# Optimization experiments

Hardware: AMD Instinct MI355X
Metric: run time of the kernel (lower is better)

The kernel has to match this reference:

```python
import jax, jax.numpy as jnp
import numpy as np

WS, SHIFT, HEADS = 8, 4, 12
B, H0, W0, C, HID = 16, 64, 64, 384, 1536
EPS = 1e-5


def _rel_pos_index():
    # WindowMSA.double_step_seq(2*Ww-1, Wh, 1, Ww), then coords + coords.T, then flip(1)
    seq1 = np.arange(0, (2 * WS - 1) * WS, 2 * WS - 1)
    seq2 = np.arange(0, WS)
    coords = (seq1[:, None] + seq2[None, :]).reshape(1, -1)  # (1, N)
    idx = coords + coords.T                                   # (N, N)
    return np.ascontiguousarray(idx[:, ::-1]).reshape(-1)

REL_IDX = jnp.asarray(_rel_pos_index())


def _attn_mask(Hp, Wp):
    # Swin shift mask: region labels -> per-window pairwise (-100 where regions differ)
    img = np.zeros((Hp, Wp))
    sl = (slice(0, -WS), slice(-WS, -SHIFT), slice(-SHIFT, None))
    cnt = 0
    for hs in sl:
        for ws in sl:
            img[hs, ws] = cnt
            cnt += 1
    mw = img.reshape(Hp // WS, WS, Wp // WS, WS).transpose(0, 2, 1, 3).reshape(-1, WS * WS)
    am = mw[:, None, :] - mw[:, :, None]
    return jnp.asarray(np.where(am != 0, -100.0, 0.0), np.float32)


def _ln(z, g, b):
    m = z.mean(-1, keepdims=True)
    v = ((z - m) ** 2).mean(-1, keepdims=True)
    return (z - m) * jax.lax.rsqrt(v + EPS) * g + b


def _bn(z, g, b):
    # eval-mode BatchNorm2d with running mean=0, var=1
    scale = g * (1.0 / np.sqrt(1.0 + EPS))
    return z * scale[None, :, None, None] + b[None, :, None, None]


def setup_inputs() -> dict:
    key = jax.random.key(0)
    ks = jax.random.split(key, 8)
    p = lambda k, sh: jax.random.normal(k, sh, jnp.float32) * 0.02
    return {
        "x": jax.random.normal(ks[0], (B, H0 * W0, C), jnp.float32),
        "H": H0, "W": W0,
        "ln1_g": jnp.ones((C,), jnp.float32), "ln1_b": jnp.zeros((C,), jnp.float32),
        "qkv_w": p(ks[1], (3 * C, C)), "qkv_b": jnp.zeros((3 * C,), jnp.float32),
        "rpb_table": p(ks[2], ((2 * WS - 1) ** 2, HEADS)),
        "proj_w": p(ks[3], (C, C)), "proj_b": jnp.zeros((C,), jnp.float32),
        "ln2_g": jnp.ones((C,), jnp.float32), "ln2_b": jnp.zeros((C,), jnp.float32),
        "fc1_w": p(ks[4], (HID, C)), "fc1_b": jnp.zeros((HID,), jnp.float32),
        "bn1_g": jnp.ones((HID,), jnp.float32), "bn1_b": jnp.zeros((HID,), jnp.float32),
        "dw_w": p(ks[5], (HID, 1, 3, 3)), "dw_b": jnp.zeros((HID,), jnp.float32),
        "bn2_g": jnp.ones((HID,), jnp.float32), "bn2_b": jnp.zeros((HID,), jnp.float32),
        "fc2_w": p(ks[6], (C, HID)), "fc2_b": jnp.zeros((C,), jnp.float32),
        "bn3_g": jnp.ones((C,), jnp.float32), "bn3_b": jnp.zeros((C,), jnp.float32),
    }


def reference(x, H, W, ln1_g, ln1_b, qkv_w, qkv_b, rpb_table, proj_w, proj_b,
              ln2_g, ln2_b, fc1_w, fc1_b, bn1_g, bn1_b, dw_w, dw_b,
              bn2_g, bn2_b, fc2_w, fc2_b, bn3_g, bn3_b):
    Bx, L, Cx = x.shape
    hd = Cx // HEADS
    # ---------- shifted-window MHSA branch ----------
    h = _ln(x, ln1_g, ln1_b).reshape(Bx, H, W, Cx)
    h = jnp.roll(h, (-SHIFT, -SHIFT), axis=(1, 2))
    nH, nW = H // WS, W // WS
    N = WS * WS
    win = h.reshape(Bx, nH, WS, nW, WS, Cx).transpose(0, 1, 3, 2, 4, 5).reshape(-1, N, Cx)
    qkv = (win @ qkv_w.T + qkv_b).reshape(-1, N, 3, HEADS, hd).transpose(2, 0, 3, 1, 4)
    q, k, v = qkv[0] * (hd ** -0.5), qkv[1], qkv[2]  # (B*nW, heads, N, hd)
    attn = jnp.einsum('whnd,whmd->whnm', q, k)
    bias = rpb_table[REL_IDX].reshape(N, N, HEADS).transpose(2, 0, 1)  # (heads, N, N)
    attn = attn + bias[None]
    mask = _attn_mask(H, W)  # (num_windows, N, N)
    attn = attn.reshape(Bx, nH * nW, HEADS, N, N) + mask[None, :, None]
    attn = jax.nn.softmax(attn.reshape(-1, HEADS, N, N), axis=-1)
    out = jnp.einsum('whnm,whmd->whnd', attn, v).transpose(0, 2, 1, 3).reshape(-1, N, Cx)
    out = out @ proj_w.T + proj_b
    out = out.reshape(Bx, nH, nW, WS, WS, Cx).transpose(0, 1, 3, 2, 4, 5).reshape(Bx, H, W, Cx)
    out = jnp.roll(out, (SHIFT, SHIFT), axis=(1, 2)).reshape(Bx, L, Cx)
    x = x + out
    # ---------- MlpDWBN branch ----------
    h = _ln(x, ln2_g, ln2_b)
    z = h.transpose(0, 2, 1).reshape(Bx, Cx, H, W)
    z = jnp.einsum('oc,bchw->bohw', fc1_w, z) + fc1_b[None, :, None, None]
    z = jax.nn.gelu(_bn(z, bn1_g, bn1_b), approximate=False)
    z = jax.lax.conv_general_dilated(z, dw_w, (1, 1), 'SAME',
                                     feature_group_count=z.shape[1],
                                     dimension_numbers=('NCHW', 'OIHW', 'NCHW'))
    z = z + dw_b[None, :, None, None]
    z = jax.nn.gelu(_bn(z, bn2_g, bn2_b), approximate=False)
    z = jnp.einsum('oc,bchw->bohw', fc2_w, z) + fc2_b[None, :, None, None]
    z = jax.nn.gelu(_bn(z, bn3_g, bn3_b), approximate=False)
    z = z.reshape(Bx, Cx, -1).transpose(0, 2, 1)
    return x + z
```

## Files before the change

kernel.cpp:

```cpp
#include <hip/hip_runtime.h>
#include <cstddef>


#define CCH 384
#define HIDCH 1536

typedef __attribute__((ext_vector_type(8))) short short8;
typedef __attribute__((ext_vector_type(4))) float f32x4;

__device__ __forceinline__ float gelu_exact(float v) {
  return 0.5f * v * (1.0f + erff(v * 0.70710678118654752440f));
}
__device__ __forceinline__ unsigned short f2bf(float f) {
  unsigned u = __builtin_bit_cast(unsigned, f);
  u = (u + 0x7FFF + ((u >> 16) & 1)) >> 16;
  return (unsigned short)u;
}
__device__ __forceinline__ float bf2f(unsigned short s) {
  return __builtin_bit_cast(float, (unsigned)s << 16);
}
__device__ __forceinline__ int region_label(int p) {
  return (p < 56) ? 0 : ((p < 60) ? 1 : 2);
}

__device__ __forceinline__ void gl_lds16(const void* g, void* l) {
  __builtin_amdgcn_global_load_lds(
      (const __attribute__((address_space(1))) unsigned int*)g,
      (__attribute__((address_space(3))) unsigned int*)l, 16, 0, 0);
}

__global__ __launch_bounds__(256) void convw_kernel(
    const float* __restrict__ a, const float* __restrict__ b,
    const float* __restrict__ c, const float* __restrict__ d,
    const float* __restrict__ dww, unsigned short* __restrict__ o,
    float* __restrict__ dwt) {
  const int i = blockIdx.x * 256 + threadIdx.x;
  if (i < 1769472) {
    float v;
    if (i < 442368) v = a[i];
    else if (i < 589824) v = b[i - 442368];
    else if (i < 1179648) v = c[i - 589824];
    else v = d[i - 1179648];
    o[i] = f2bf(v);
  } else if (i < 1769472 + 13824) {
    const int j = i - 1769472;
    const int tap = j / 1536;
    const int ch = j - tap * 1536;
    dwt[j] = dww[ch * 9 + tap];
  }
}

template <int REMAP>
__global__ __launch_bounds__(256) void ln_kernel(const float* __restrict__ x,
                                                 const float* __restrict__ g,
                                                 const float* __restrict__ b,
                                                 unsigned short* __restrict__ y) {
  const int t = blockIdx.x * 4 + (threadIdx.x >> 6);
  const int lane = threadIdx.x & 63;
  size_t src;
  if (REMAP) {
    const int widx = t >> 6;
    const int n = t & 63;
    const int bb = widx >> 6;
    const int wh = (widx >> 3) & 7;
    const int ww = widx & 7;
    const int hp = wh * 8 + (n >> 3);
    const int wp = ww * 8 + (n & 7);
    const int hs = (hp + 4) & 63;
    const int wsrc = (wp + 4) & 63;
    src = (size_t)bb * 4096 + hs * 64 + wsrc;
  } else {
    src = (size_t)t;
  }
  const float* xr = x + src * CCH + lane * 6;
  const float2 p0 = *(const float2*)xr;
  const float2 p1 = *(const float2*)(xr + 2);
  const float2 p2 = *(const float2*)(xr + 4);
  float v[6] = {p0.x, p0.y, p1.x, p1.y, p2.x, p2.y};
  float s = 0.f, s2 = 0.f;
#pragma unroll
  for (int j = 0; j < 6; ++j) {
    s += v[j];
    s2 += v[j] * v[j];
  }
#pragma unroll
  for (int o = 1; o < 64; o <<= 1) {
    s += __shfl_xor(s, o);
    s2 += __shfl_xor(s2, o);
  }
  const float mean = s * (1.0f / 384.0f);
  const float var = s2 * (1.0f / 384.0f) - mean * mean;
  const float rstd = rsqrtf(var + 1e-5f);
  const float2 g0 = *(const float2*)(g + lane * 6);
  const float2 g1 = *(const float2*)(g + lane * 6 + 2);
  const float2 g2 = *(const float2*)(g + lane * 6 + 4);
  const float2 b0 = *(const float2*)(b + lane * 6);
  const float2 b1 = *(const float2*)(b + lane * 6 + 2);
  const float2 b2 = *(const float2*)(b + lane * 6 + 4);
  const float gg[6] = {g0.x, g0.y, g1.x, g1.y, g2.x, g2.y};
  const float bv[6] = {b0.x, b0.y, b1.x, b1.y, b2.x, b2.y};
  unsigned pk[3];
#pragma unroll
  for (int i = 0; i < 3; ++i) {
    const float r0 = (v[2 * i] - mean) * rstd * gg[2 * i] + bv[2 * i];
    const float r1 = (v[2 * i + 1] - mean) * rstd * gg[2 * i + 1] + bv[2 * i + 1];
    pk[i] = (unsigned)f2bf(r0) | ((unsigned)f2bf(r1) << 16);
  }
  unsigned* yo = (unsigned*)(y + (size_t)t * CCH + lane * 6);
  yo[0] = pk[0];
  yo[1] = pk[1];
  yo[2] = pk[2];
}

template <int MODE>
__global__ __launch_bounds__(512) void mfma_gemm(
    const unsigned short* __restrict__ A, const unsigned short* __restrict__ W,
    const float* __restrict__ bias, void* __restrict__ CoutV,
    const float* __restrict__ Xres, const float* __restrict__ bng,
    const float* __restrict__ bnb, int N, int K) {
  __shared__ __align__(16) char smem[32768];
  const int tid = threadIdx.x;
  const int wave = tid >> 6, lane = tid & 63;
  const int qd = lane >> 4, ln16 = lane & 15;
  const int wm = wave >> 2, wn = wave & 3;

  const int nx = gridDim.x;
  const int lid0 = blockIdx.x + blockIdx.y * nx;
  const int tot = nx * gridDim.y;
  int lid = lid0;
  if ((tot & 7) == 0) lid = (lid0 & 7) * (tot >> 3) + (lid0 >> 3);
  const int m0 = (lid % nx) * 128;
  const int n0 = (lid / nx) * 128;

  f32x4 acc[4][2];
#pragma unroll
  for (int i = 0; i < 4; ++i)
#pragma unroll
    for (int j = 0; j < 2; ++j) acc[i][j] = (f32x4){0.f, 0.f, 0.f, 0.f};

  const int r = tid >> 2;
  const int cks = ((tid & 3) ^ ((tid >> 3) & 3)) * 8;

  const unsigned short* gA = A + (size_t)(m0 + r) * K + cks;
  const unsigned short* gB = W + (size_t)(n0 + r) * K + cks;
  char* baseA = smem;
  char* baseB = smem + 16384;
  const int wofs = wave * 1024;

  const int ntk = K >> 5;
  gl_lds16(gA, baseA + wofs);
  gl_lds16(gB, baseB + wofs);

  const int sA = (qd ^ ((ln16 >> 1) & 3)) * 8;

  int cur = 0;
  for (int t = 0; t < ntk; ++t) {
    __builtin_amdgcn_s_barrier();
    __builtin_amdgcn_sched_barrier(0);
    if (t + 1 < ntk) {
      const int k1 = (t + 1) * 32;
      const int nb = cur ^ 1;
      gl_lds16(gA + k1, baseA + nb * 8192 + wofs);
      gl_lds16(gB + k1, baseB + nb * 8192 + wofs);
      asm volatile("s_waitcnt vmcnt(2)" ::: "memory");
    } else {
      asm volatile("s_waitcnt vmcnt(0)" ::: "memory");
    }
    __builtin_amdgcn_s_barrier();
    __builtin_amdgcn_sched_barrier(0);
    short8 af[4], bfr[2];
#pragma unroll
    for (int mt = 0; mt < 4; ++mt)
      af[mt] = *(const short8*)(baseA + cur * 8192 +
                                ((wm * 64 + mt * 16 + ln16) * 32 + sA) * 2);
#pragma unroll
    for (int nt2 = 0; nt2 < 2; ++nt2)
      bfr[nt2] = *(const short8*)(baseB + cur * 8192 +
                                  ((wn * 32 + nt2 * 16 + ln16) * 32 + sA) * 2);
#pragma unroll
    for (int mt = 0; mt < 4; ++mt)
#pragma unroll
      for (int nt2 = 0; nt2 < 2; ++nt2)
        acc[mt][nt2] = __builtin_amdgcn_mfma_f32_16x16x32_bf16(
            af[mt], bfr[nt2], acc[mt][nt2], 0, 0, 0);
    cur ^= 1;
  }

  const float RSQ = 0.99999500003749969f;
#pragma unroll
  for (int mt = 0; mt < 4; ++mt) {
#pragma unroll
    for (int nt2 = 0; nt2 < 2; ++nt2) {
      const int col = n0 + wn * 32 + nt2 * 16 + ln16;
      const int rbase = m0 + wm * 64 + mt * 16 + qd * 4;
#pragma unroll
      for (int rg = 0; rg < 4; ++rg) {
        const int row = rbase + rg;
        const float val = acc[mt][nt2][rg] + bias[col];
        if (MODE == 0) {
          ((unsigned short*)CoutV)[(size_t)row * N + col] = f2bf(val);
        } else if (MODE == 1) {
          const int widx = row >> 6, n = row & 63;
          const int bb = widx >> 6, wh = (widx >> 3) & 7, wwi = widx & 7;
          const int hp = wh * 8 + (n >> 3), wp = wwi * 8 + (n & 7);
          const int hh = (hp + 4) & 63, wwp = (wp + 4) & 63;
          const size_t dst = ((size_t)bb * 4096 + hh * 64 + wwp) * CCH + col;
          ((float*)CoutV)[dst] = Xres[dst] + val;
        } else {
          const float vbn = val * (bng[col] * RSQ) + bnb[col];
          const float ge = gelu_exact(vbn);
          if (MODE == 2) {
            ((unsigned short*)CoutV)[(size_t)row * N + col] = f2bf(ge);
          } else {
            float* o = (float*)CoutV + (size_t)row * N + col;
            *o = *o + ge;
          }
        }
      }
    }
  }
}

__global__ __launch_bounds__(256) void attn_kernel(
    const unsigned short* __restrict__ qkv, const float* __restrict__ rpb,
    unsigned short* __restrict__ ao) {
  __shared__ __align__(16) unsigned short Pl[4][64 * 72];
  __shared__ float Inv[4][64];
  const int wloc = blockIdx.x;
  const int wave = threadIdx.x >> 6;
  const int lane = threadIdx.x & 63;
  const int head = blockIdx.y * 4 + wave;
  const int ln16 = lane & 15, qd = lane >> 4;
  const int wpos = wloc & 63;
  const int wh = (wpos >> 3) & 7, ww = wpos & 7;
  const unsigned short* qb = qkv + (size_t)wloc * 64 * 1152 + head * 32;

  short8 aq[4], bk[4];
#pragma unroll
  for (int t = 0; t < 4; ++t) {
    aq[t] = *(const short8*)(qb + (size_t)(t * 16 + ln16) * 1152 + qd * 8);
    bk[t] = *(const short8*)(qb + (size_t)(t * 16 + ln16) * 1152 + 384 + qd * 8);
  }
  short8 av[2][2];
#pragma unroll
  for (int dt = 0; dt < 2; ++dt)
#pragma unroll
    for (int ks = 0; ks < 2; ++ks)
#pragma unroll
      for (int j = 0; j < 8; ++j)
        av[dt][ks][j] = (short)qb[(size_t)(ks * 32 + qd * 8 + j) * 1152 + 768 +
                                  dt * 16 + ln16];

  f32x4 accS[4][4];
#pragma unroll
  for (int i = 0; i < 4; ++i)
#pragma unroll
    for (int j = 0; j < 4; ++j) accS[i][j] = (f32x4){0.f, 0.f, 0.f, 0.f};
#pragma unroll
  for (int mt = 0; mt < 4; ++mt)
#pragma unroll
    for (int nt = 0; nt < 4; ++nt)
      accS[mt][nt] = __builtin_amdgcn_mfma_f32_16x16x32_bf16(
          aq[mt], bk[nt], accS[mt][nt], 0, 0, 0);

  int cmv[4], rlm[4];
#pragma unroll
  for (int nt = 0; nt < 4; ++nt) {
    const int m = nt * 16 + ln16;
    const int mf = 63 - m;
    cmv[nt] = 15 * (mf >> 3) + (mf & 7);
    rlm[nt] =
        region_label(wh * 8 + (m >> 3)) * 3 + region_label(ww * 8 + (m & 7));
  }
  const float scale = 0.17677669529663687f;
  unsigned short* pw = &Pl[wave][0];
#pragma unroll
  for (int mt = 0; mt < 4; ++mt) {
#pragma unroll
    for (int rg = 0; rg < 4; ++rg) {
      const int n = mt * 16 + qd * 4 + rg;
      const int cn = 15 * (n >> 3) + (n & 7);
      const int rln =
          region_label(wh * 8 + (n >> 3)) * 3 + region_label(ww * 8 + (n & 7));
      float vv[4];
#pragma unroll
      for (int nt = 0; nt < 4; ++nt) {
        float sv = accS[mt][nt][rg] * scale + rpb[(cn + cmv[nt]) * 12 + head];
        if (rln != rlm[nt]) sv -= 100.f;
        vv[nt] = sv;
      }
      float mx = fmaxf(fmaxf(vv[0], vv[1]), fmaxf(vv[2], vv[3]));
      mx = fmaxf(mx, __shfl_xor(mx, 1));
      mx = fmaxf(mx, __shfl_xor(mx, 2));
      mx = fmaxf(mx, __shfl_xor(mx, 4));
      mx = fmaxf(mx, __shfl_xor(mx, 8));
      float sum = 0.f;
#pragma unroll
      for (int nt = 0; nt < 4; ++nt) {
        vv[nt] = __expf(vv[nt] - mx);
        sum += vv[nt];
      }
      sum += __shfl_xor(sum, 1);
      sum += __shfl_xor(sum, 2);
      sum += __shfl_xor(sum, 4);
      sum += __shfl_xor(sum, 8);
      if (ln16 == 0) Inv[wave][n] = 1.0f / sum;
#pragma unroll
      for (int nt = 0; nt < 4; ++nt)
        pw[n * 72 + nt * 16 + ln16] = f2bf(vv[nt]);
    }
  }

  f32x4 accO[2][4];
#pragma unroll
  for (int i = 0; i < 2; ++i)
#pragma unroll
    for (int j = 0; j < 4; ++j) accO[i][j] = (f32x4){0.f, 0.f, 0.f, 0.f};
#pragma unroll
  for (int ks = 0; ks < 2; ++ks) {
    short8 pb[4];
#pragma unroll
    for (int ntile = 0; ntile < 4; ++ntile)
      pb[ntile] =
          *(const short8*)&pw[(ntile * 16 + ln16) * 72 + ks * 32 + qd * 8];
#pragma unroll
    for (int dt = 0; dt < 2; ++dt)
#pragma unroll
      for (int ntile = 0; ntile < 4; ++ntile)
        accO[dt][ntile] = __builtin_amdgcn_mfma_f32_16x16x32_bf16(
            av[dt][ks], pb[ntile], accO[dt][ntile], 0, 0, 0);
  }

  float invn[4];
#pragma unroll
  for (int ntile = 0; ntile < 4; ++ntile)
    invn[ntile] = Inv[wave][ntile * 16 + ln16];
#pragma unroll
  for (int dt = 0; dt < 2; ++dt) {
#pragma unroll
    for (int ntile = 0; ntile < 4; ++ntile) {
      const int tok = ntile * 16 + ln16;
      const int d0 = dt * 16 + qd * 4;
      uint2 st;
      st.x = (unsigned)f2bf(accO[dt][ntile][0] * invn[ntile]) |
             ((unsigned)f2bf(accO[dt][ntile][1] * invn[ntile]) << 16);
      st.y = (unsigned)f2bf(accO[dt][ntile][2] * invn[ntile]) |
             ((unsigned)f2bf(accO[dt][ntile][3] * invn[ntile]) << 16);
      *(uint2*)&ao[((size_t)wloc * 64 + tok) * CCH + head * 32 + d0] = st;
    }
  }
}

__global__ __launch_bounds__(256) void dw_kernel(
    const unsigned short* __restrict__ z1, const float* __restrict__ dwt,
    const float* __restrict__ dwb, const float* __restrict__ bn2g,
    const float* __restrict__ bn2b, unsigned short* __restrict__ z2) {
  const int g = blockIdx.x * 256 + threadIdx.x;
  const int pix = g / 192;
  const int cg = g - pix * 192;
  const int c0 = cg * 8;
  const int p = pix & 4095;
  const int h = p >> 6, w = p & 63;
  const unsigned short* zb = z1 + (size_t)(pix >> 12) * 4096 * HIDCH;

  float a[8];
  {
    const float4 b0 = *(const float4*)&dwb[c0];
    const float4 b1 = *(const float4*)&dwb[c0 + 4];
    a[0] = b0.x; a[1] = b0.y; a[2] = b0.z; a[3] = b0.w;
    a[4] = b1.x; a[5] = b1.y; a[6] = b1.z; a[7] = b1.w;
  }
#pragma unroll
  for (int dh = -1; dh <= 1; ++dh) {
    const int hh = h + dh;
    if (hh < 0 || hh > 63) continue;
#pragma unroll
    for (int dx = -1; dx <= 1; ++dx) {
      const int wn = w + dx;
      if (wn < 0 || wn > 63) continue;
      const int tap = (dh + 1) * 3 + (dx + 1);
      const int4 zv = *(const int4*)&zb[((size_t)hh * 64 + wn) * HIDCH + c0];
      const float* wp = &dwt[tap * HIDCH + c0];
      const float4 w0 = *(const float4*)wp;
      const float4 w1 = *(const float4*)(wp + 4);
      a[0] += bf2f((unsigned short)(zv.x & 0xFFFF)) * w0.x;
      a[1] += bf2f((unsigned short)(((unsigned)zv.x) >> 16)) * w0.y;
      a[2] += bf2f((unsigned short)(zv.y & 0xFFFF)) * w0.z;
      a[3] += bf2f((unsigned short)(((unsigned)zv.y) >> 16)) * w0.w;
      a[4] += bf2f((unsigned short)(zv.z & 0xFFFF)) * w1.x;
      a[5] += bf2f((unsigned short)(((unsigned)zv.z) >> 16)) * w1.y;
      a[6] += bf2f((unsigned short)(zv.w & 0xFFFF)) * w1.z;
      a[7] += bf2f((unsigned short)(((unsigned)zv.w) >> 16)) * w1.w;
    }
  }
  const float RSQ = 0.99999500003749969f;
  const float4 g0 = *(const float4*)&bn2g[c0];
  const float4 g1 = *(const float4*)&bn2g[c0 + 4];
  const float4 bb0 = *(const float4*)&bn2b[c0];
  const float4 bb1 = *(const float4*)&bn2b[c0 + 4];
  const float gs[8] = {g0.x, g0.y, g0.z, g0.w, g1.x, g1.y, g1.z, g1.w};
  const float bs[8] = {bb0.x, bb0.y, bb0.z, bb0.w, bb1.x, bb1.y, bb1.z, bb1.w};
  unsigned pk[4];
#pragma unroll
  for (int i = 0; i < 4; ++i) {
    const float v0 = gelu_exact(a[2 * i] * (gs[2 * i] * RSQ) + bs[2 * i]);
    const float v1 =
        gelu_exact(a[2 * i + 1] * (gs[2 * i + 1] * RSQ) + bs[2 * i + 1]);
    pk[i] = (unsigned)f2bf(v0) | ((unsigned)f2bf(v1) << 16);
  }
  int4 st;
  st.x = pk[0]; st.y = pk[1]; st.z = pk[2]; st.w = pk[3];
  *(int4*)&z2[(size_t)pix * HIDCH + c0] = st;
}

extern "C" void kernel_launch(void* const* d_in, const int* in_sizes, int n_in,
                              void* d_out, int out_size, void* d_ws,
                              size_t ws_size, hipStream_t stream) {
  const float* x = (const float*)d_in[0];
  const float* ln1_g = (const float*)d_in[3];
  const float* ln1_b = (const float*)d_in[4];
  const float* qkv_w = (const float*)d_in[5];
  const float* qkv_b = (const float*)d_in[6];
  const float* rpb = (const float*)d_in[7];
  const float* proj_w = (const float*)d_in[8];
  const float* proj_b = (const float*)d_in[9];
  const float* ln2_g = (const float*)d_in[10];
  const float* ln2_b = (const float*)d_in[11];
  const float* fc1_w = (const float*)d_in[12];
  const float* fc1_b = (const float*)d_in[13];
  const float* bn1_g = (const float*)d_in[14];
  const float* bn1_b = (const float*)d_in[15];
  const float* dw_w = (const float*)d_in[16];
  const float* dw_b = (const float*)d_in[17];
  const float* bn2_g = (const float*)d_in[18];
  const float* bn2_b = (const float*)d_in[19];
  const float* fc2_w = (const float*)d_in[20];
  const float* fc2_b = (const float*)d_in[21];
  const float* bn3_g = (const float*)d_in[22];
  const float* bn3_b = (const float*)d_in[23];
  float* out = (float*)d_out;

  char* ws = (char*)d_ws;
  unsigned short* wsA = (unsigned short*)ws;
  unsigned short* wsAO = (unsigned short*)(ws + 50331648);
  unsigned short* wsQ = (unsigned short*)(ws + 100663296);
  unsigned short* wbf = (unsigned short*)(ws + 150994944);
  float* dwt = (float*)(ws + 154533888);
  unsigned short* w_qkv = wbf;
  unsigned short* w_proj = wbf + 442368;
  unsigned short* w_fc1 = wbf + 589824;
  unsigned short* w_fc2 = wbf + 1179648;

  convw_kernel<<<6966, 256, 0, stream>>>(qkv_w, proj_w, fc1_w, fc2_w, dw_w,
                                         wbf, dwt);
  ln_kernel<1><<<16384, 256, 0, stream>>>(x, ln1_g, ln1_b, wsA);
  for (int cb = 0; cb < 4; ++cb) {
    mfma_gemm<0><<<dim3(128, 9), 512, 0, stream>>>(
        wsA + (size_t)cb * 16384 * CCH, w_qkv, qkv_b, wsQ, nullptr, nullptr,
        nullptr, 1152, CCH);
    attn_kernel<<<dim3(256, 3), 256, 0, stream>>>(
        wsQ, rpb, wsAO + (size_t)cb * 16384 * CCH);
  }
  mfma_gemm<1><<<dim3(512, 3), 512, 0, stream>>>(wsAO, w_proj, proj_b, out, x,
                                                 nullptr, nullptr, CCH, CCH);
  ln_kernel<0><<<16384, 256, 0, stream>>>(out, ln2_g, ln2_b, wsA);
  for (int cb = 0; cb < 4; ++cb) {
    mfma_gemm<2><<<dim3(128, 12), 512, 0, stream>>>(
        wsA + (size_t)cb * 16384 * CCH, w_fc1, fc1_b, wsAO, nullptr, bn1_g,
        bn1_b, HIDCH, CCH);
    dw_kernel<<<12288, 256, 0, stream>>>(wsAO, dwt, dw_b, bn2_g, bn2_b, wsQ);
    mfma_gemm<3><<<dim3(128, 3), 512, 0, stream>>>(
        wsQ, w_fc2, fc2_b, out + (size_t)cb * 16384 * CCH, nullptr, bn3_g,
        bn3_b, CCH, HIDCH);
  }
}
```

Baseline: 1.071 ms.

## Fuse proj GEMM with residual and LayerNorm2; deepen GEMM K-step to 64

Replaces the separate projection GEMM and the second LayerNorm kernel with a single kernel. Each block computes 64 full rows of 384 outputs, adds the residual, reduces row statistics across waves through shared memory, and writes both the fp32 output and the bf16 normalized activations. This removes one full read of the activation tensor and one kernel launch. Separately, the generic MFMA GEMM now stages K=64 per iteration with a 64KB double-buffered LDS and a new XOR swizzle, halving the number of barrier rounds. In exchange, the larger LDS footprint may lower occupancy, and the LN variance is computed as E[x²]−mean², which is less numerically robust.

```diff
diff --git a/kernel.cpp b/kernel.cpp
--- a/kernel.cpp
+++ b/kernel.cpp
@@ -116,9 +116,9 @@
 __global__ __launch_bounds__(512) void mfma_gemm(
     const unsigned short* __restrict__ A, const unsigned short* __restrict__ W,
     const float* __restrict__ bias, void* __restrict__ CoutV,
-    const float* __restrict__ Xres, const float* __restrict__ bng,
-    const float* __restrict__ bnb, int N, int K) {
-  __shared__ __align__(16) char smem[32768];
+    const float* __restrict__ bng, const float* __restrict__ bnb, int N,
+    int K) {
+  __shared__ __align__(16) char smem[65536];
   const int tid = threadIdx.x;
   const int wave = tid >> 6, lane = tid & 63;
   const int qd = lane >> 4, ln16 = lane & 15;
@@ -138,51 +138,63 @@
 #pragma unroll
     for (int j = 0; j < 2; ++j) acc[i][j] = (f32x4){0.f, 0.f, 0.f, 0.f};
 
-  const int r = tid >> 2;
-  const int cks = ((tid & 3) ^ ((tid >> 3) & 3)) * 8;
-
-  const unsigned short* gA = A + (size_t)(m0 + r) * K + cks;
-  const unsigned short* gB = W + (size_t)(n0 + r) * K + cks;
-  char* baseA = smem;
-  char* baseB = smem + 16384;
+  const int rowg = tid >> 3;
+  const int cswz = ((tid & 7) ^ (rowg & 7)) * 8;
+  const unsigned short* gA = A + (size_t)(m0 + rowg) * K + cswz;
+  const unsigned short* gB = W + (size_t)(n0 + rowg) * K + cswz;
+  const size_t rstep = (size_t)64 * K;
   const int wofs = wave * 1024;
 
-  const int ntk = K >> 5;
-  gl_lds16(gA, baseA + wofs);
-  gl_lds16(gB, baseB + wofs);
-
-  const int sA = (qd ^ ((ln16 >> 1) & 3)) * 8;
+  const int ntk = K >> 6;
+  gl_lds16(gA, smem + wofs);
+  gl_lds16(gA + rstep, smem + 8192 + wofs);
+  gl_lds16(gB, smem + 16384 + wofs);
+  gl_lds16(gB + rstep, smem + 24576 + wofs);
 
   int cur = 0;
   for (int t = 0; t < ntk; ++t) {
     __builtin_amdgcn_s_barrier();
     __builtin_amdgcn_sched_barrier(0);
     if (t + 1 < ntk) {
-      const int k1 = (t + 1) * 32;
-      const int nb = cur ^ 1;
-      gl_lds16(gA + k1, baseA + nb * 8192 + wofs);
-      gl_lds16(gB + k1, baseB + nb * 8192 + wofs);
-      asm volatile("s_waitcnt vmcnt(2)" ::: "memory");
+      const int k1 = (t + 1) * 64;
+      char* nb = smem + (cur ^ 1) * 32768;
+      gl_lds16(gA + k1, nb + wofs);
+      gl_lds16(gA + rstep + k1, nb + 8192 + wofs);
+      gl_lds16(gB + k1, nb + 16384 + wofs);
+      gl_lds16(gB + rstep + k1, nb + 24576 + wofs);
+      asm volatile("s_waitcnt vmcnt(4)" ::: "memory");
     } else {
       asm volatile("s_waitcnt vmcnt(0)" ::: "memory");
     }
     __builtin_amdgcn_s_barrier();
     __builtin_amdgcn_sched_barrier(0);
-    short8 af[4], bfr[2];
-#pragma unroll
-    for (int mt = 0; mt < 4; ++mt)
-      af[mt] = *(const short8*)(baseA + cur * 8192 +
-                                ((wm * 64 + mt * 16 + ln16) * 32 + sA) * 2);
-#pragma unroll
-    for (int nt2 = 0; nt2 < 2; ++nt2)
-      bfr[nt2] = *(const short8*)(baseB + cur * 8192 +
-                                  ((wn * 32 + nt2 * 16 + ln16) * 32 + sA) * 2);
-#pragma unroll
-    for (int mt = 0; mt < 4; ++mt)
-#pragma unroll
-      for (int nt2 = 0; nt2 < 2; ++nt2)
-        acc[mt][nt2] = __builtin_amdgcn_mfma_f32_16x16x32_bf16(
-            af[mt], bfr[nt2], acc[mt][nt2], 0, 0, 0);
+    const char* bA = smem + cur * 32768;
+    const char* bB = bA + 16384;
+    short8 af[4][2], bfr[2][2];
+#pragma unroll
+    for (int mt = 0; mt < 4; ++mt) {
+      const int row = wm * 64 + mt * 16 + ln16;
+#pragma unroll
+      for (int kk = 0; kk < 2; ++kk)
+        af[mt][kk] = *(const short8*)(bA + row * 128 +
+                                      (((kk << 2) + qd) ^ (ln16 & 7)) * 16);
+    }
+#pragma unroll
+    for (int nt2 = 0; nt2 < 2; ++nt2) {
+      const int row = wn * 32 + nt2 * 16 + ln16;
+#pragma unroll
+      for (int kk = 0; kk < 2; ++kk)
+        bfr[nt2][kk] = *(const short8*)(bB + row * 128 +
+                                        (((kk << 2) + qd) ^ (ln16 & 7)) * 16);
+    }
+#pragma unroll
+    for (int kk = 0; kk < 2; ++kk)
+#pragma unroll
+      for (int mt = 0; mt < 4; ++mt)
+#pragma unroll
+        for (int nt2 = 0; nt2 < 2; ++nt2)
+          acc[mt][nt2] = __builtin_amdgcn_mfma_f32_16x16x32_bf16(
+              af[mt][kk], bfr[nt2][kk], acc[mt][nt2], 0, 0, 0);
     cur ^= 1;
   }
 
@@ -199,13 +211,6 @@
         const float val = acc[mt][nt2][rg] + bias[col];
         if (MODE == 0) {
           ((unsigned short*)CoutV)[(size_t)row * N + col] = f2bf(val);
-        } else if (MODE == 1) {
-          const int widx = row >> 6, n = row & 63;
-          const int bb = widx >> 6, wh = (widx >> 3) & 7, wwi = widx & 7;
-          const int hp = wh * 8 + (n >> 3), wp = wwi * 8 + (n & 7);
-          const int hh = (hp + 4) & 63, wwp = (wp + 4) & 63;
-          const size_t dst = ((size_t)bb * 4096 + hh * 64 + wwp) * CCH + col;
-          ((float*)CoutV)[dst] = Xres[dst] + val;
         } else {
           const float vbn = val * (bng[col] * RSQ) + bnb[col];
           const float ge = gelu_exact(vbn);
@@ -216,6 +221,142 @@
             *o = *o + ge;
           }
         }
+      }
+    }
+  }
+}
+
+__global__ __launch_bounds__(512) void proj_ln_kernel(
+    const unsigned short* __restrict__ A, const unsigned short* __restrict__ W,
+    const float* __restrict__ bias, float* __restrict__ out,
+    const float* __restrict__ Xres, const float* __restrict__ lng,
+    const float* __restrict__ lnb, unsigned short* __restrict__ y) {
+  __shared__ __align__(16) char smem[65536];
+  const int tid = threadIdx.x;
+  const int wave = tid >> 6, lane = tid & 63;
+  const int qd = lane >> 4, ln16 = lane & 15;
+  const int wm = wave >> 2, wn = wave & 3;
+
+  const int tot = gridDim.x;
+  int lid = blockIdx.x;
+  if ((tot & 7) == 0) lid = (lid & 7) * (tot >> 3) + (lid >> 3);
+  const int m0 = lid * 64;
+
+  f32x4 acc[2][6];
+#pragma unroll
+  for (int i = 0; i < 2; ++i)
+#pragma unroll
+    for (int j = 0; j < 6; ++j) acc[i][j] = (f32x4){0.f, 0.f, 0.f, 0.f};
+
+  const int srow = tid >> 2;
+  const int s = tid & 3;
+  const unsigned short* gp[4];
+#pragma unroll
+  for (int c = 0; c < 4; ++c) {
+    const int R = c * 128 + srow;
+    const int sw = (s ^ ((R >> 1) & 3)) * 8;
+    if (R < 384)
+      gp[c] = W + (size_t)R * CCH + sw;
+    else
+      gp[c] = A + (size_t)(m0 + ((R - 384) & 63)) * CCH + sw;
+  }
+  const int wofs = wave * 1024;
+
+#pragma unroll
+  for (int c = 0; c < 4; ++c) gl_lds16(gp[c], smem + c * 8192 + wofs);
+
+  int cur = 0;
+  for (int t = 0; t < 12; ++t) {
+    __builtin_amdgcn_s_barrier();
+    __builtin_amdgcn_sched_barrier(0);
+    if (t + 1 < 12) {
+      const int k1 = (t + 1) * 32;
+      char* nb = smem + (cur ^ 1) * 32768;
+#pragma unroll
+      for (int c = 0; c < 4; ++c) gl_lds16(gp[c] + k1, nb + c * 8192 + wofs);
+      asm volatile("s_waitcnt vmcnt(4)" ::: "memory");
+    } else {
+      asm volatile("s_waitcnt vmcnt(0)" ::: "memory");
+    }
+    __builtin_amdgcn_s_barrier();
+    __builtin_amdgcn_sched_barrier(0);
+    const char* bb = smem + cur * 32768;
+    short8 af[2], bfr[6];
+#pragma unroll
+    for (int mt = 0; mt < 2; ++mt) {
+      const int row = 384 + wm * 32 + mt * 16 + ln16;
+      af[mt] = *(const short8*)(bb + row * 64 + (qd ^ ((row >> 1) & 3)) * 16);
+    }
+#pragma unroll
+    for (int nt = 0; nt < 6; ++nt) {
+      const int row = wn * 96 + nt * 16 + ln16;
+      bfr[nt] = *(const short8*)(bb + row * 64 + (qd ^ ((row >> 1) & 3)) * 16);
+    }
+#pragma unroll
+    for (int mt = 0; mt < 2; ++mt)
+#pragma unroll
+      for (int nt = 0; nt < 6; ++nt)
+        acc[mt][nt] = __builtin_amdgcn_mfma_f32_16x16x32_bf16(
+            af[mt], bfr[nt], acc[mt][nt], 0, 0, 0);
+    cur ^= 1;
+  }
+
+  const int bb_ = lid >> 6, wh = (lid >> 3) & 7, wwi = lid & 7;
+  float* stats = (float*)smem;
+#pragma unroll
+  for (int mt = 0; mt < 2; ++mt) {
+#pragma unroll
+    for (int rg = 0; rg < 4; ++rg) {
+      const int rloc = wm * 32 + mt * 16 + qd * 4 + rg;
+      const int hp = wh * 8 + (rloc >> 3), wp = wwi * 8 + (rloc & 7);
+      const int hh = (hp + 4) & 63, wwp = (wp + 4) & 63;
+      const size_t drow = ((size_t)bb_ * 4096 + hh * 64 + wwp) * CCH;
+      float sv = 0.f, sv2 = 0.f;
+#pragma unroll
+      for (int nt = 0; nt < 6; ++nt) {
+        const int col = wn * 96 + nt * 16 + ln16;
+        const float o = Xres[drow + col] + acc[mt][nt][rg] + bias[col];
+        out[drow + col] = o;
+        acc[mt][nt][rg] = o;
+        sv += o;
+        sv2 += o * o;
+      }
+      sv += __shfl_xor(sv, 1);
+      sv2 += __shfl_xor(sv2, 1);
+      sv += __shfl_xor(sv, 2);
+      sv2 += __shfl_xor(sv2, 2);
+      sv += __shfl_xor(sv, 4);
+      sv2 += __shfl_xor(sv2, 4);
+      sv += __shfl_xor(sv, 8);
+      sv2 += __shfl_xor(sv2, 8);
+      if (ln16 == 0) {
+        stats[rloc * 8 + wn * 2] = sv;
+        stats[rloc * 8 + wn * 2 + 1] = sv2;
+      }
+    }
+  }
+  __syncthreads();
+#pragma unroll
+  for (int mt = 0; mt < 2; ++mt) {
+#pragma unroll
+    for (int rg = 0; rg < 4; ++rg) {
+      const int rloc = wm * 32 + mt * 16 + qd * 4 + rg;
+      const float ts = stats[rloc * 8 + 0] + stats[rloc * 8 + 2] +
+                       stats[rloc * 8 + 4] + stats[rloc * 8 + 6];
+      const float ts2 = stats[rloc * 8 + 1] + stats[rloc * 8 + 3] +
+                        stats[rloc * 8 + 5] + stats[rloc * 8 + 7];
+      const float mean = ts * (1.0f / 384.0f);
+      const float var = ts2 * (1.0f / 384.0f) - mean * mean;
+      const float rstd = rsqrtf(var + 1e-5f);
+      const int hp = wh * 8 + (rloc >> 3), wp = wwi * 8 + (rloc & 7);
+      const int hh = (hp + 4) & 63, wwp = (wp + 4) & 63;
+      const size_t drow = ((size_t)bb_ * 4096 + hh * 64 + wwp) * CCH;
+#pragma unroll
+      for (int nt = 0; nt < 6; ++nt) {
+        const int col = wn * 96 + nt * 16 + ln16;
+        const float yv =
+            (acc[mt][nt][rg] - mean) * rstd * lng[col] + lnb[col];
+        y[drow + col] = f2bf(yv);
       }
     }
   }
@@ -457,20 +598,19 @@
   for (int cb = 0; cb < 4; ++cb) {
     mfma_gemm<0><<<dim3(128, 9), 512, 0, stream>>>(
         wsA + (size_t)cb * 16384 * CCH, w_qkv, qkv_b, wsQ, nullptr, nullptr,
-        nullptr, 1152, CCH);
+        1152, CCH);
     attn_kernel<<<dim3(256, 3), 256, 0, stream>>>(
         wsQ, rpb, wsAO + (size_t)cb * 16384 * CCH);
   }
-  mfma_gemm<1><<<dim3(512, 3), 512, 0, stream>>>(wsAO, w_proj, proj_b, out, x,
-                                                 nullptr, nullptr, CCH, CCH);
-  ln_kernel<0><<<16384, 256, 0, stream>>>(out, ln2_g, ln2_b, wsA);
+  proj_ln_kernel<<<1024, 512, 0, stream>>>(wsAO, w_proj, proj_b, out, x,
+                                           ln2_g, ln2_b, wsA);
   for (int cb = 0; cb < 4; ++cb) {
     mfma_gemm<2><<<dim3(128, 12), 512, 0, stream>>>(
-        wsA + (size_t)cb * 16384 * CCH, w_fc1, fc1_b, wsAO, nullptr, bn1_g,
-        bn1_b, HIDCH, CCH);
+        wsA + (size_t)cb * 16384 * CCH, w_fc1, fc1_b, wsAO, bn1_g, bn1_b,
+        HIDCH, CCH);
     dw_kernel<<<12288, 256, 0, stream>>>(wsAO, dwt, dw_b, bn2_g, bn2_b, wsQ);
     mfma_gemm<3><<<dim3(128, 3), 512, 0, stream>>>(
-        wsQ, w_fc2, fc2_b, out + (size_t)cb * 16384 * CCH, nullptr, bn3_g,
-        bn3_b, CCH, HIDCH);
-  }
-}
+        wsQ, w_fc2, fc2_b, out + (size_t)cb * 16384 * CCH, bn3_g, bn3_b, CCH,
+        HIDCH);
+  }
+}
```

Measured after the change: 1.112 ms. 1.04x slower.
